# Kernel tuning notes

Measured on AMD Instinct MI355X. Metric: run time of the kernel, lower is better.

Reference implementation:

```python
import jax, jax.numpy as jnp
import numpy as np
from jax import lax

B, T, V, D, H, NH = 32, 2048, 50257, 512, 512, 2
HD = D // NH
EPS_ATTN = 1e-6
EPS_LN = 1e-5


def setup_inputs() -> dict:
    key = jax.random.key(0)
    ks = jax.random.split(key, 16)
    s = 0.02
    n = lambda k, shape: jax.random.normal(k, shape, jnp.float32) * s
    return {
        'input_ids': jax.random.randint(ks[0], (B, T), 0, V),
        'emb': n(ks[1], (V, D)),
        'Wq': n(ks[2], (D, D)), 'Wk': n(ks[3], (D, D)), 'Wv': n(ks[4], (D, D)),
        'Wo': n(ks[5], (D, D)),  # present in module, unused in forward (kept for parity)
        'Wg': n(ks[6], (D, D)), 'bg': jnp.zeros((D,), jnp.float32),
        'W_in': n(ks[7], (H, D)), 'b_in': jnp.zeros((H,), jnp.float32),
        'W_h': n(ks[8], (H, H)),
        'log_tau': jnp.zeros((H,), jnp.float32),
        'log_dt': jnp.zeros((H,), jnp.float32),
        'W_zx': n(ks[9], (H, D)), 'b_zx': jnp.zeros((H,), jnp.float32),
        'W_zh': n(ks[10], (H, H)),
        'fast_W': jnp.zeros((H, H), jnp.float32),  # registered buffer, starts at zero
        'ln_g': jnp.ones((H,), jnp.float32), 'ln_b': jnp.zeros((H,), jnp.float32),
        'Wlm': n(ks[11], (V, H)), 'blm': jnp.zeros((V,), jnp.float32),
    }


def _phi(x):
    return jax.nn.elu(x) + 1.0


def _forward(input_ids, emb, Wq, Wk, Wv, Wo, Wg, bg, W_in, b_in, W_h, log_tau,
             log_dt, W_zx, b_zx, W_zh, fast_W, ln_g, ln_b, Wlm, blm):
    x = emb[input_ids]  # [B,T,D]

    # LiquidSelfAttention (diagonal linear attention, as written in the source)
    q = _phi((x @ Wq.T).reshape(B, T, NH, HD))
    k = _phi((x @ Wk.T).reshape(B, T, NH, HD))
    v = (x @ Wv.T).reshape(B, T, NH, HD)
    k_sum = k.sum(axis=1)                       # [B,NH,HD]
    kv_sum = (k * v).sum(axis=1)                # einsum('bthd,bthd->bhd')
    num = jnp.einsum('bthd,bhd->bth', q, kv_sum)[..., None]   # [B,T,NH,1]
    den = jnp.einsum('bthd,bhd->bth', q, k_sum)[..., None] + EPS_ATTN
    out = jnp.broadcast_to(num / den, (B, T, NH, HD)).reshape(B, T, D)
    gate = jax.nn.sigmoid(x @ Wg.T + bg)
    x = gate * out + (1.0 - gate) * x           # [B,T,D]

    # Liquid-GRU recurrence with fast-weight term
    tau = jnp.exp(log_tau)
    dt = jnp.exp(log_dt)
    h0 = jnp.zeros((B, H), x.dtype)

    def step(carry, x_t):
        h, _ = carry
        u = x_t @ W_in.T + b_in + h @ W_h.T
        f = jnp.tanh(u)
        h_liquid = h + dt * (f - tau * h)
        z = jax.nn.sigmoid(x_t @ W_zx.T + b_zx + h @ W_zh.T)
        slow_h = (1.0 - z) * h + z * h_liquid
        h_next = slow_h + h @ fast_W
        return (h_next, h), None

    (h_last, h_prev), _ = lax.scan(step, (h0, h0), jnp.swapaxes(x, 0, 1))
    pred_error = h_last - h_prev  # last-step prediction error (T >= 2)

    # LayerNorm (dropout is identity in eval)
    mu = h_last.mean(axis=-1, keepdims=True)
    var = ((h_last - mu) ** 2).mean(axis=-1, keepdims=True)
    h = (h_last - mu) * lax.rsqrt(var + EPS_LN) * ln_g + ln_b

    logits = h @ Wlm.T + blm
    pred_error_norm = jnp.sqrt(jnp.mean(pred_error ** 2))
    return logits, h, pred_error_norm


def reference(input_ids, emb, Wq, Wk, Wv, Wo, Wg, bg, W_in, b_in, W_h, log_tau,
              log_dt, W_zx, b_zx, W_zh, fast_W, ln_g, ln_b, Wlm, blm):
    return _forward(input_ids, emb, Wq, Wk, Wv, Wo, Wg, bg, W_in, b_in, W_h,
                    log_tau, log_dt, W_zx, b_zx, W_zh, fast_W, ln_g, ln_b, Wlm, blm)
```

## Files before the change

### kernel.cpp

```cpp
#include <hip/hip_runtime.h>
#include <cstdint>
#include <cstddef>


#define B_ 32
#define T_ 2048
#define V_ 50257
#define D_ 512
#define H_ 512
#define NH_ 2
#define BT_ (B_*T_)

typedef float f32x4 __attribute__((ext_vector_type(4)));

#define OFF_X0    ((size_t)0)
#define OFF_X1    (OFF_X0 + (size_t)BT_*D_*4)
#define OFF_XZ    (OFF_X1 + (size_t)BT_*D_*4)
#define OFF_SMALL (OFF_XZ + (size_t)BT_*D_*4)
#define OFF_RBUF  (OFF_SMALL)
#define OFF_KSUM  (OFF_RBUF + (size_t)BT_*NH_*2*4)
#define OFF_KVSUM (OFF_KSUM + (size_t)B_*D_*4)
#define OFF_FLAGS (OFF_KVSUM + (size_t)B_*D_*4)
#define OFF_HBUF  (OFF_FLAGS + 16384)
#define OFF_HLN   (OFF_HBUF + (size_t)2*B_*H_*4)
#define ZERO_F4   ((OFF_HBUF - OFF_SMALL) / 16)

__device__ __forceinline__ float phi_f(float x) {
  return x > 0.f ? x + 1.f : expf(x);
}
__device__ __forceinline__ float sigm_f(float x) {
  return 1.f / (1.f + expf(-x));
}

__global__ __launch_bounds__(256) void zero_k(float4* __restrict__ p, int n) {
  int i = blockIdx.x * 256 + threadIdx.x;
  if (i < n) p[i] = make_float4(0.f, 0.f, 0.f, 0.f);
}

__global__ __launch_bounds__(256) void fillnan_k(uint4* __restrict__ p) {
  size_t i = (size_t)blockIdx.x * 256 + threadIdx.x;
  uint4 v;
  v.x = 0x7FC00000u; v.y = 0x7FC00000u; v.z = 0x7FC00000u; v.w = 0x7FC00000u;
  p[i] = v;
}

__global__ __launch_bounds__(256) void embed_k(const int* __restrict__ ids,
                                               const float* __restrict__ emb,
                                               float* __restrict__ x0) {
  size_t idx = (size_t)blockIdx.x * 256 + threadIdx.x;
  int row = (int)(idx >> 7), c = (int)(idx & 127);
  int id = ids[row];
  ((float4*)x0)[idx] = ((const float4*)emb)[(size_t)id * 128 + c];
}

template<int MODE>
__global__ __launch_bounds__(256, 2) void gemm_k(
    const float* __restrict__ X, const float* __restrict__ W0,
    const float* __restrict__ W1, const float* __restrict__ bias,
    const float* __restrict__ aux0, const float* __restrict__ aux1,
    float* __restrict__ out0, float* __restrict__ out1) {
  constexpr bool KV = (MODE == 0);
  __shared__ float Xs[32][68];
  __shared__ float Ws[32][68];
  __shared__ float Ws2[KV ? 32 : 1][68];
  const int tid = threadIdx.x;
  const int m0 = blockIdx.x * 64, n0 = blockIdx.y * 64;
  const int tm = tid >> 4, tn = tid & 15;
  const int lr = tid >> 3;
  const int lc = (tid & 7) * 4;
  float acc[4][4] = {};
  float acc2[KV ? 4 : 1][4] = {};

  for (int k0 = 0; k0 < 512; k0 += 32) {
    const float4 xa = *(const float4*)&X[(size_t)(m0 + lr) * 512 + k0 + lc];
    const float4 xb = *(const float4*)&X[(size_t)(m0 + 32 + lr) * 512 + k0 + lc];
    const float4 wa = *(const float4*)&W0[(size_t)(n0 + lr) * 512 + k0 + lc];
    const float4 wb = *(const float4*)&W0[(size_t)(n0 + 32 + lr) * 512 + k0 + lc];
    float4 va, vb;
    if constexpr (KV) {
      va = *(const float4*)&W1[(size_t)(n0 + lr) * 512 + k0 + lc];
      vb = *(const float4*)&W1[(size_t)(n0 + 32 + lr) * 512 + k0 + lc];
    }
    __syncthreads();
    Xs[lc+0][lr] = xa.x; Xs[lc+1][lr] = xa.y; Xs[lc+2][lr] = xa.z; Xs[lc+3][lr] = xa.w;
    Xs[lc+0][lr+32] = xb.x; Xs[lc+1][lr+32] = xb.y; Xs[lc+2][lr+32] = xb.z; Xs[lc+3][lr+32] = xb.w;
    Ws[lc+0][lr] = wa.x; Ws[lc+1][lr] = wa.y; Ws[lc+2][lr] = wa.z; Ws[lc+3][lr] = wa.w;
    Ws[lc+0][lr+32] = wb.x; Ws[lc+1][lr+32] = wb.y; Ws[lc+2][lr+32] = wb.z; Ws[lc+3][lr+32] = wb.w;
    if constexpr (KV) {
      Ws2[lc+0][lr] = va.x; Ws2[lc+1][lr] = va.y; Ws2[lc+2][lr] = va.z; Ws2[lc+3][lr] = va.w;
      Ws2[lc+0][lr+32] = vb.x; Ws2[lc+1][lr+32] = vb.y; Ws2[lc+2][lr+32] = vb.z; Ws2[lc+3][lr+32] = vb.w;
    }
    __syncthreads();
    #pragma unroll
    for (int kk = 0; kk < 32; ++kk) {
      float4 xv = *(const float4*)&Xs[kk][tm * 4];
      float4 wv = *(const float4*)&Ws[kk][tn * 4];
      const float* xf = (const float*)&xv;
      const float* wf = (const float*)&wv;
      #pragma unroll
      for (int i = 0; i < 4; ++i)
        #pragma unroll
        for (int j = 0; j < 4; ++j)
          acc[i][j] += xf[i] * wf[j];
      if constexpr (KV) {
        float4 wv2 = *(const float4*)&Ws2[kk][tn * 4];
        const float* w2 = (const float*)&wv2;
        #pragma unroll
        for (int i = 0; i < 4; ++i)
          #pragma unroll
          for (int j = 0; j < 4; ++j)
            acc2[i][j] += xf[i] * w2[j];
      }
    }
  }

  if constexpr (MODE == 0) {
    __syncthreads();
    float* red = &Xs[0][0];
    if (tid < 128) red[tid] = 0.f;
    __syncthreads();
    #pragma unroll
    for (int j = 0; j < 4; ++j) {
      float ks = 0.f, kvs = 0.f;
      #pragma unroll
      for (int i = 0; i < 4; ++i) {
        float kk_ = phi_f(acc[i][j]);
        ks += kk_;
        kvs += kk_ * acc2[i][j];
      }
      atomicAdd(&red[(tn * 4 + j) * 2 + 0], ks);
      atomicAdd(&red[(tn * 4 + j) * 2 + 1], kvs);
    }
    __syncthreads();
    if (tid < 64) {
      int b = m0 >> 11;
      atomicAdd(&out0[b * 512 + n0 + tid], red[tid * 2 + 0]);
      atomicAdd(&out1[b * 512 + n0 + tid], red[tid * 2 + 1]);
    }
  } else if constexpr (MODE == 1) {
    int b = m0 >> 11;
    float kvv[4], ksv[4];
    #pragma unroll
    for (int j = 0; j < 4; ++j) {
      int n = n0 + tn * 4 + j;
      kvv[j] = aux0[b * 512 + n];
      ksv[j] = aux1[b * 512 + n];
    }
    __syncthreads();
    float* red = &Xs[0][0];
    if (tid < 128) red[tid] = 0.f;
    __syncthreads();
    #pragma unroll
    for (int i = 0; i < 4; ++i) {
      float np = 0.f, dp = 0.f;
      #pragma unroll
      for (int j = 0; j < 4; ++j) {
        float q = phi_f(acc[i][j]);
        np += q * kvv[j];
        dp += q * ksv[j];
      }
      atomicAdd(&red[(tm * 4 + i) * 2 + 0], np);
      atomicAdd(&red[(tm * 4 + i) * 2 + 1], dp);
    }
    __syncthreads();
    if (tid < 64) {
      int m = m0 + tid, h = n0 >> 8;
      atomicAdd(&out0[((size_t)m * 2 + h) * 2 + 0], red[tid * 2 + 0]);
      atomicAdd(&out0[((size_t)m * 2 + h) * 2 + 1], red[tid * 2 + 1]);
    }
  } else if constexpr (MODE == 2) {
    int h = n0 >> 8;
    #pragma unroll
    for (int i = 0; i < 4; ++i) {
      int m = m0 + tm * 4 + i;
      float rn = aux0[((size_t)m * 2 + h) * 2 + 0];
      float rd = aux0[((size_t)m * 2 + h) * 2 + 1];
      float r = rn / (rd + 1e-6f);
      float4 x0v = *(const float4*)&aux1[(size_t)m * 512 + n0 + tn * 4];
      const float* xf = (const float*)&x0v;
      float4 o;
      float* of = (float*)&o;
      #pragma unroll
      for (int j = 0; j < 4; ++j) {
        int n = n0 + tn * 4 + j;
        float g = sigm_f(acc[i][j] + bias[n]);
        of[j] = g * r + (1.f - g) * xf[j];
      }
      *(float4*)&out0[(size_t)m * 512 + n0 + tn * 4] = o;
    }
  } else {
    #pragma unroll
    for (int i = 0; i < 4; ++i) {
      int m = m0 + tm * 4 + i;
      float4 o;
      float* of = (float*)&o;
      #pragma unroll
      for (int j = 0; j < 4; ++j)
        of[j] = acc[i][j] + bias[n0 + tn * 4 + j];
      *(float4*)&out0[(size_t)m * 512 + n0 + tn * 4] = o;
    }
  }
}


#define ISSUE8(h0,h1,h2,h3,h4_,h5,h6,h7,ptr) \
  asm volatile( \
    "global_load_dwordx4 %0, %8, off sc0 sc1\n\t" \
    "global_load_dwordx4 %1, %8, off offset:16 sc0 sc1\n\t" \
    "global_load_dwordx4 %2, %8, off offset:32 sc0 sc1\n\t" \
    "global_load_dwordx4 %3, %8, off offset:48 sc0 sc1\n\t" \
    "global_load_dwordx4 %4, %8, off offset:64 sc0 sc1\n\t" \
    "global_load_dwordx4 %5, %8, off offset:80 sc0 sc1\n\t" \
    "global_load_dwordx4 %6, %8, off offset:96 sc0 sc1\n\t" \
    "global_load_dwordx4 %7, %8, off offset:112 sc0 sc1" \
    : "=v"(h0), "=v"(h1), "=v"(h2), "=v"(h3), \
      "=v"(h4_), "=v"(h5), "=v"(h6), "=v"(h7) \
    : "v"(ptr))

#define WAIT_TIE(h0,h1,h2,h3,h4_,h5,h6,h7) \
  asm volatile("s_waitcnt vmcnt(0)" \
    : "+v"(h0), "+v"(h1), "+v"(h2), "+v"(h3), \
      "+v"(h4_), "+v"(h5), "+v"(h6), "+v"(h7))

__global__ __launch_bounds__(1024) void scan_k(
    const float* __restrict__ xin, const float* __restrict__ xz,
    const float* __restrict__ Wh, const float* __restrict__ Wzh,
    const float* __restrict__ fastW,
    const float* __restrict__ log_tau, const float* __restrict__ log_dt,
    float* __restrict__ hist) {
  __shared__ float red[16][64][3];
  __shared__ __align__(16) float h_lds[2][64];
  const int tid = threadIdx.x;
  const int b = blockIdx.x >> 3;
  const int q = blockIdx.x & 7;
  const int w = tid >> 6;
  const int lane = tid & 63;
  const int jg = q * 64 + lane;
  const int kb = w * 32;
  const int src = w >> 1;

  f32x4 wh[8], wz[8], fw[8];
  #pragma unroll
  for (int i = 0; i < 8; ++i) {
    wh[i] = *(const f32x4*)&Wh[(size_t)jg * 512 + kb + i * 4];
    wz[i] = *(const f32x4*)&Wzh[(size_t)jg * 512 + kb + i * 4];
    f32x4 tv;
    tv.x = fastW[(size_t)(kb + i * 4 + 0) * 512 + jg];
    tv.y = fastW[(size_t)(kb + i * 4 + 1) * 512 + jg];
    tv.z = fastW[(size_t)(kb + i * 4 + 2) * 512 + jg];
    tv.w = fastW[(size_t)(kb + i * 4 + 3) * 512 + jg];
    fw[i] = tv;
  }
  bool fwz = true;
  #pragma unroll
  for (int i = 0; i < 8; ++i)
    fwz = fwz & (fw[i].x == 0.f) & (fw[i].y == 0.f) & (fw[i].z == 0.f) & (fw[i].w == 0.f);

  const float dtv = expf(log_dt[jg]);
  const float tauv = expf(log_tau[jg]);
  float hold = 0.f;
  float pxin = 0.f, pxz = 0.f;
  if (w == 0) {
    const float* xip = xin + (size_t)b * T_ * 512 + jg;
    const float* xzp = xz + (size_t)b * T_ * 512 + jg;
    asm volatile("global_load_dword %0, %2, off\n\t"
                 "global_load_dword %1, %3, off"
                 : "=v"(pxin), "=v"(pxz) : "v"(xip), "v"(xzp));
  }

  for (int t = 0; t < T_; ++t) {
    float am0 = 0.f, am1 = 0.f, am2 = 0.f;
    if (t != 0) {
      f32x4 hv[8];
      if (src == q) {
        const float* hl = &h_lds[t & 1][kb & 63];
        #pragma unroll
        for (int i = 0; i < 8; ++i) hv[i] = *(const f32x4*)(hl + i * 4);
      } else {
        const float* hp = hist + (size_t)(t - 1) * (B_ * H_) + b * 512 + kb;
        ISSUE8(hv[0], hv[1], hv[2], hv[3], hv[4], hv[5], hv[6], hv[7], hp);
        while (true) {
          WAIT_TIE(hv[0], hv[1], hv[2], hv[3], hv[4], hv[5], hv[6], hv[7]);
          f32x4 sv = hv[0] + hv[1] + hv[2] + hv[3] + hv[4] + hv[5] + hv[6] + hv[7];
          float sred = sv.x + sv.y + sv.z + sv.w;
          if ((__float_as_uint(sred) & 0x7F800000u) != 0x7F800000u) break;
          ISSUE8(hv[0], hv[1], hv[2], hv[3], hv[4], hv[5], hv[6], hv[7], hp);
        }
      }
      #pragma unroll
      for (int i = 0; i < 8; ++i) {
        f32x4 h4 = hv[i];
        am0 += wh[i].x * h4.x + wh[i].y * h4.y + wh[i].z * h4.z + wh[i].w * h4.w;
        am1 += wz[i].x * h4.x + wz[i].y * h4.y + wz[i].z * h4.z + wz[i].w * h4.w;
      }
      if (!fwz) {
        #pragma unroll
        for (int i = 0; i < 8; ++i) {
          f32x4 h4 = hv[i];
          am2 += fw[i].x * h4.x + fw[i].y * h4.y + fw[i].z * h4.z + fw[i].w * h4.w;
        }
      }
    }
    red[w][lane][0] = am0;
    red[w][lane][1] = am1;
    red[w][lane][2] = am2;
    __syncthreads();
    if (w == 0) {
      float s0 = 0.f, s1 = 0.f, s2 = 0.f;
      #pragma unroll
      for (int ww = 0; ww < 16; ++ww) {
        s0 += red[ww][lane][0];
        s1 += red[ww][lane][1];
        s2 += red[ww][lane][2];
      }
      asm volatile("s_waitcnt vmcnt(0)" : "+v"(pxin), "+v"(pxz));
      float u = pxin + s0;
      float f = tanhf(u);
      float hl2 = hold + dtv * (f - tauv * hold);
      float zv = sigm_f(pxz + s1);
      float slow = (1.f - zv) * hold + zv * hl2;
      float hnv = slow + s2;
      hold = hnv;
      h_lds[(t + 1) & 1][lane] = hnv;
      float* dst = hist + (size_t)t * (B_ * H_) + b * 512 + jg;
      asm volatile("global_store_dword %0, %1, off sc0 sc1" :: "v"(dst), "v"(hnv) : "memory");
      if (t + 1 < T_) {
        const float* xip = xin + ((size_t)b * T_ + (t + 1)) * 512 + jg;
        const float* xzp = xz + ((size_t)b * T_ + (t + 1)) * 512 + jg;
        asm volatile("global_load_dword %0, %2, off\n\t"
                     "global_load_dword %1, %3, off"
                     : "=v"(pxin), "=v"(pxz) : "v"(xip), "v"(xzp));
      }
    }
    __syncthreads();
  }
}

__global__ __launch_bounds__(256) void pred_k(const float* __restrict__ hA,
                                              const float* __restrict__ hB,
                                              float* __restrict__ out) {
  const int tid = threadIdx.x;
  float s = 0.f;
  for (int i = tid; i < H_ * B_; i += 256) {
    float a = __hip_atomic_load((const float*)&hA[i], __ATOMIC_RELAXED, __HIP_MEMORY_SCOPE_AGENT);
    float b = __hip_atomic_load((const float*)&hB[i], __ATOMIC_RELAXED, __HIP_MEMORY_SCOPE_AGENT);
    float d = a - b;
    s += d * d;
  }
  #pragma unroll
  for (int m = 1; m < 64; m <<= 1) s += __shfl_xor(s, m, 64);
  __shared__ float r8[4];
  if ((tid & 63) == 0) r8[tid >> 6] = s;
  __syncthreads();
  if (tid == 0) out[0] = sqrtf((r8[0] + r8[1] + r8[2] + r8[3]) * (1.f / (H_ * B_)));
}

__global__ __launch_bounds__(256) void ln_k(const float* __restrict__ h0,
                                            const float* __restrict__ g,
                                            const float* __restrict__ be,
                                            float* __restrict__ hln,
                                            float* __restrict__ outh) {
  const int b = blockIdx.x, tid = threadIdx.x;
  float v0 = __hip_atomic_load((const float*)&h0[b * 512 + tid], __ATOMIC_RELAXED, __HIP_MEMORY_SCOPE_AGENT);
  float v1 = __hip_atomic_load((const float*)&h0[b * 512 + tid + 256], __ATOMIC_RELAXED, __HIP_MEMORY_SCOPE_AGENT);
  float s = v0 + v1;
  #pragma unroll
  for (int m = 1; m < 64; m <<= 1) s += __shfl_xor(s, m, 64);
  __shared__ float r8[8];
  if ((tid & 63) == 0) r8[tid >> 6] = s;
  __syncthreads();
  float mu = (r8[0] + r8[1] + r8[2] + r8[3]) * (1.f / 512.f);
  float d0 = v0 - mu, d1 = v1 - mu;
  float s2 = d0 * d0 + d1 * d1;
  #pragma unroll
  for (int m = 1; m < 64; m <<= 1) s2 += __shfl_xor(s2, m, 64);
  if ((tid & 63) == 0) r8[4 + (tid >> 6)] = s2;
  __syncthreads();
  float var = (r8[4] + r8[5] + r8[6] + r8[7]) * (1.f / 512.f);
  float inv = rsqrtf(var + 1e-5f);
  float y0 = d0 * inv * g[tid] + be[tid];
  float y1 = d1 * inv * g[tid + 256] + be[tid + 256];
  hln[b * 512 + tid] = y0;
  hln[b * 512 + tid + 256] = y1;
  outh[b * 512 + tid] = y0;
  outh[b * 512 + tid + 256] = y1;
}

__global__ __launch_bounds__(256, 2) void logits_k(const float* __restrict__ hln,
                                                   const float* __restrict__ Wlm,
                                                   const float* __restrict__ blm,
                                                   float* __restrict__ out) {
  __shared__ float hs[32 * 513];
  const int tid = threadIdx.x;
  for (int idx = tid; idx < 16384; idx += 256) {
    int b = idx >> 9, k = idx & 511;
    hs[b * 513 + k] = hln[idx];
  }
  __syncthreads();
  const int lane = tid & 63, w = tid >> 6;
  const int b = lane & 31, kh = lane >> 5;
  const float* hb = &hs[b * 513 + kh * 256];
  const int vbase = blockIdx.x * 64 + w * 16;
  for (int r4 = 0; r4 < 16; r4 += 4) {
    int v = vbase + r4;
    int v0i = (v + 0 < V_) ? v + 0 : V_ - 1;
    int v1i = (v + 1 < V_) ? v + 1 : V_ - 1;
    int v2i = (v + 2 < V_) ? v + 2 : V_ - 1;
    int v3i = (v + 3 < V_) ? v + 3 : V_ - 1;
    const float4* w0 = (const float4*)&Wlm[(size_t)v0i * 512 + kh * 256];
    const float4* w1 = (const float4*)&Wlm[(size_t)v1i * 512 + kh * 256];
    const float4* w2 = (const float4*)&Wlm[(size_t)v2i * 512 + kh * 256];
    const float4* w3 = (const float4*)&Wlm[(size_t)v3i * 512 + kh * 256];
    float a0 = 0.f, a1 = 0.f, a2 = 0.f, a3 = 0.f;
    #pragma unroll 8
    for (int q = 0; q < 64; ++q) {
      float h0 = hb[q * 4 + 0], h1 = hb[q * 4 + 1], h2 = hb[q * 4 + 2], h3 = hb[q * 4 + 3];
      float4 x;
      x = w0[q]; a0 += x.x * h0 + x.y * h1 + x.z * h2 + x.w * h3;
      x = w1[q]; a1 += x.x * h0 + x.y * h1 + x.z * h2 + x.w * h3;
      x = w2[q]; a2 += x.x * h0 + x.y * h1 + x.z * h2 + x.w * h3;
      x = w3[q]; a3 += x.x * h0 + x.y * h1 + x.z * h2 + x.w * h3;
    }
    a0 += __shfl_xor(a0, 32, 64);
    a1 += __shfl_xor(a1, 32, 64);
    a2 += __shfl_xor(a2, 32, 64);
    a3 += __shfl_xor(a3, 32, 64);
    if (lane < 32) {
      if (v + 0 < V_) out[(size_t)b * V_ + v + 0] = a0 + blm[v + 0];
      if (v + 1 < V_) out[(size_t)b * V_ + v + 1] = a1 + blm[v + 1];
      if (v + 2 < V_) out[(size_t)b * V_ + v + 2] = a2 + blm[v + 2];
      if (v + 3 < V_) out[(size_t)b * V_ + v + 3] = a3 + blm[v + 3];
    }
  }
}

extern "C" void kernel_launch(void* const* d_in, const int* in_sizes, int n_in,
                              void* d_out, int out_size, void* d_ws, size_t ws_size,
                              hipStream_t stream) {
  const int*   ids     = (const int*)d_in[0];
  const float* emb     = (const float*)d_in[1];
  const float* Wq      = (const float*)d_in[2];
  const float* Wk      = (const float*)d_in[3];
  const float* Wv      = (const float*)d_in[4];
  const float* Wg      = (const float*)d_in[6];
  const float* bg      = (const float*)d_in[7];
  const float* W_in    = (const float*)d_in[8];
  const float* b_in    = (const float*)d_in[9];
  const float* W_h     = (const float*)d_in[10];
  const float* log_tau = (const float*)d_in[11];
  const float* log_dt  = (const float*)d_in[12];
  const float* W_zx    = (const float*)d_in[13];
  const float* b_zx    = (const float*)d_in[14];
  const float* W_zh    = (const float*)d_in[15];
  const float* fast_W  = (const float*)d_in[16];
  const float* ln_g    = (const float*)d_in[17];
  const float* ln_b    = (const float*)d_in[18];
  const float* Wlm     = (const float*)d_in[19];
  const float* blm     = (const float*)d_in[20];

  char* ws = (char*)d_ws;
  float* x0    = (float*)(ws + OFF_X0);
  float* x1    = (float*)(ws + OFF_X1);
  float* xzb   = (float*)(ws + OFF_XZ);
  float* rbuf  = (float*)(ws + OFF_RBUF);
  float* ksum  = (float*)(ws + OFF_KSUM);
  float* kvsum = (float*)(ws + OFF_KVSUM);
  float* hln   = (float*)(ws + OFF_HLN);
  float* out   = (float*)d_out;

  const int nzero = (int)ZERO_F4;
  zero_k<<<dim3((nzero + 255) / 256), dim3(256), 0, stream>>>((float4*)(ws + OFF_SMALL), nzero);
  embed_k<<<dim3(BT_ * 128 / 256), dim3(256), 0, stream>>>(ids, emb, x0);

  dim3 gg(BT_ / 64, 8);
  gemm_k<0><<<gg, dim3(256), 0, stream>>>(x0, Wk, Wv, nullptr, nullptr, nullptr, ksum, kvsum);
  gemm_k<1><<<gg, dim3(256), 0, stream>>>(x0, Wq, nullptr, nullptr, kvsum, ksum, rbuf, nullptr);
  gemm_k<2><<<gg, dim3(256), 0, stream>>>(x0, Wg, nullptr, bg, rbuf, x0, x1, nullptr);
  gemm_k<3><<<gg, dim3(256), 0, stream>>>(x1, W_in, nullptr, b_in, nullptr, nullptr, x0, nullptr);
  gemm_k<3><<<gg, dim3(256), 0, stream>>>(x1, W_zx, nullptr, b_zx, nullptr, nullptr, xzb, nullptr);

  fillnan_k<<<dim3(BT_ * D_ / 4 / 256), dim3(256), 0, stream>>>((uint4*)x1);

  scan_k<<<dim3(256), dim3(1024), 0, stream>>>(x0, xzb, W_h, W_zh, fast_W, log_tau, log_dt, x1);

  float* hlast = x1 + (size_t)2047 * (B_ * H_);
  float* hprev = x1 + (size_t)2046 * (B_ * H_);
  pred_k<<<dim3(1), dim3(256), 0, stream>>>(hlast, hprev, out + (size_t)B_ * V_ + (size_t)B_ * H_);
  ln_k<<<dim3(32), dim3(256), 0, stream>>>(hlast, ln_g, ln_b, hln, out + (size_t)B_ * V_);
  logits_k<<<dim3((V_ + 63) / 64), dim3(256), 0, stream>>>(hln, Wlm, blm, out);
}
```

Measured before the change: 7.691 ms.

## Exchange partial matvec sums via triple-buffered slots instead of full hidden-state history

```diff
diff --git a/kernel.cpp b/kernel.cpp
--- a/kernel.cpp
+++ b/kernel.cpp
@@ -25,6 +25,9 @@
 #define OFF_HLN   (OFF_HBUF + (size_t)2*B_*H_*4)
 #define ZERO_F4   ((OFF_HBUF - OFF_SMALL) / 16)
 
+#define MATS_MAX 3
+#define SLOT_F   (MATS_MAX*8*512)
+
 __device__ __forceinline__ float phi_f(float x) {
   return x > 0.f ? x + 1.f : expf(x);
 }
@@ -42,6 +45,13 @@
   uint4 v;
   v.x = 0x7FC00000u; v.y = 0x7FC00000u; v.z = 0x7FC00000u; v.w = 0x7FC00000u;
   p[i] = v;
+}
+
+__global__ __launch_bounds__(256) void fwnz_k(const float* __restrict__ fw,
+                                              int* __restrict__ flag) {
+  int i = (blockIdx.x * 256 + threadIdx.x) * 4;
+  float4 v = *(const float4*)&fw[i];
+  if (v.x != 0.f || v.y != 0.f || v.z != 0.f || v.w != 0.f) atomicOr(flag, 1);
 }
 
 __global__ __launch_bounds__(256) void embed_k(const int* __restrict__ ids,
@@ -203,117 +213,87 @@
 }
 
 
-#define ISSUE8(h0,h1,h2,h3,h4_,h5,h6,h7,ptr) \
-  asm volatile( \
-    "global_load_dwordx4 %0, %8, off sc0 sc1\n\t" \
-    "global_load_dwordx4 %1, %8, off offset:16 sc0 sc1\n\t" \
-    "global_load_dwordx4 %2, %8, off offset:32 sc0 sc1\n\t" \
-    "global_load_dwordx4 %3, %8, off offset:48 sc0 sc1\n\t" \
-    "global_load_dwordx4 %4, %8, off offset:64 sc0 sc1\n\t" \
-    "global_load_dwordx4 %5, %8, off offset:80 sc0 sc1\n\t" \
-    "global_load_dwordx4 %6, %8, off offset:96 sc0 sc1\n\t" \
-    "global_load_dwordx4 %7, %8, off offset:112 sc0 sc1" \
-    : "=v"(h0), "=v"(h1), "=v"(h2), "=v"(h3), \
-      "=v"(h4_), "=v"(h5), "=v"(h6), "=v"(h7) \
-    : "v"(ptr))
-
-#define WAIT_TIE(h0,h1,h2,h3,h4_,h5,h6,h7) \
-  asm volatile("s_waitcnt vmcnt(0)" \
-    : "+v"(h0), "+v"(h1), "+v"(h2), "+v"(h3), \
-      "+v"(h4_), "+v"(h5), "+v"(h6), "+v"(h7))
+#define LOADWAIT(dst, ptr) \
+  asm volatile("global_load_dword %0, %1, off sc0 sc1\n\t" \
+               "s_waitcnt vmcnt(0)" \
+               : "=v"(dst) : "v"(ptr) : "memory")
+#define PSTORE(ptr, val) \
+  asm volatile("global_store_dword %0, %1, off sc0 sc1" :: "v"(ptr), "v"(val) : "memory")
 
 __global__ __launch_bounds__(1024) void scan_k(
     const float* __restrict__ xin, const float* __restrict__ xz,
     const float* __restrict__ Wh, const float* __restrict__ Wzh,
     const float* __restrict__ fastW,
     const float* __restrict__ log_tau, const float* __restrict__ log_dt,
-    float* __restrict__ hist) {
-  __shared__ float red[16][64][3];
-  __shared__ __align__(16) float h_lds[2][64];
+    float* __restrict__ slots, float* __restrict__ hlast,
+    float* __restrict__ hprev, const int* __restrict__ fwflag) {
+  __shared__ float red[24][64];
+  __shared__ __align__(16) float h_lds[64];
   const int tid = threadIdx.x;
   const int b = blockIdx.x >> 3;
-  const int q = blockIdx.x & 7;
-  const int w = tid >> 6;
-  const int lane = tid & 63;
-  const int jg = q * 64 + lane;
-  const int kb = w * 32;
-  const int src = w >> 1;
-
-  f32x4 wh[8], wz[8], fw[8];
+  const int o = blockIdx.x & 7;
+  const int w = tid >> 6, lane = tid & 63;
+  const int j = tid & 511, mat = tid >> 9;
+  const int mats = (fwflag[0] != 0) ? 3 : 2;
+
+  const float* Wsel = mat ? Wzh : Wh;
+  f32x4 wv[16];
   #pragma unroll
-  for (int i = 0; i < 8; ++i) {
-    wh[i] = *(const f32x4*)&Wh[(size_t)jg * 512 + kb + i * 4];
-    wz[i] = *(const f32x4*)&Wzh[(size_t)jg * 512 + kb + i * 4];
-    f32x4 tv;
-    tv.x = fastW[(size_t)(kb + i * 4 + 0) * 512 + jg];
-    tv.y = fastW[(size_t)(kb + i * 4 + 1) * 512 + jg];
-    tv.z = fastW[(size_t)(kb + i * 4 + 2) * 512 + jg];
-    tv.w = fastW[(size_t)(kb + i * 4 + 3) * 512 + jg];
-    fw[i] = tv;
-  }
-  bool fwz = true;
-  #pragma unroll
-  for (int i = 0; i < 8; ++i)
-    fwz = fwz & (fw[i].x == 0.f) & (fw[i].y == 0.f) & (fw[i].z == 0.f) & (fw[i].w == 0.f);
-
-  const float dtv = expf(log_dt[jg]);
-  const float tauv = expf(log_tau[jg]);
-  float hold = 0.f;
-  float pxin = 0.f, pxz = 0.f;
+  for (int i = 0; i < 16; ++i)
+    wv[i] = *(const f32x4*)&Wsel[(size_t)j * 512 + o * 64 + i * 4];
+
+  const int col = o * 64 + lane;
+  const float* xinb = xin + (size_t)b * T_ * 512 + col;
+  const float* xzbp = xz + (size_t)b * T_ * 512 + col;
+  float dtv = 0.f, tauv = 0.f, hold = 0.f, pxin = 0.f, pxz = 0.f;
   if (w == 0) {
-    const float* xip = xin + (size_t)b * T_ * 512 + jg;
-    const float* xzp = xz + (size_t)b * T_ * 512 + jg;
-    asm volatile("global_load_dword %0, %2, off\n\t"
-                 "global_load_dword %1, %3, off"
-                 : "=v"(pxin), "=v"(pxz) : "v"(xip), "v"(xzp));
-  }
+    dtv = expf(log_dt[col]);
+    tauv = expf(log_tau[col]);
+    pxin = xinb[0];
+    pxz = xzbp[0];
+  }
+
+  const float qnan = __int_as_float(0x7FC00000);
 
   for (int t = 0; t < T_; ++t) {
-    float am0 = 0.f, am1 = 0.f, am2 = 0.f;
     if (t != 0) {
-      f32x4 hv[8];
-      if (src == q) {
-        const float* hl = &h_lds[t & 1][kb & 63];
+      const float* base = slots + ((size_t)(t % 3) * 32 + b) * SLOT_F;
+      const float* cp = base + w * 512 + col;
+      float pv;
+      while (true) {
+        LOADWAIT(pv, cp);
+        if (__ballot((__float_as_uint(pv) & 0x7F800000u) != 0x7F800000u) == ~0ull) break;
+      }
+      red[w][lane] = pv;
+      if (mats == 3 && w < 8) {
+        const float* cp2 = base + (16 + w) * 512 + col;
+        float pv2;
+        while (true) {
+          LOADWAIT(pv2, cp2);
+          if (__ballot((__float_as_uint(pv2) & 0x7F800000u) != 0x7F800000u) == ~0ull) break;
+        }
+        red[16 + w][lane] = pv2;
+      }
+    } else {
+      red[w][lane] = 0.f;
+      if (mats == 3 && w < 8) red[16 + w][lane] = 0.f;
+    }
+    __syncthreads();
+
+    float* nfb = slots + ((size_t)((t + 2) % 3) * 32 + b) * SLOT_F;
+    if (w != 0) {
+      if (t >= 1) {
+        PSTORE(nfb + (mat * 8 + o) * 512 + j, qnan);
+        if (mats == 3 && mat == 0) PSTORE(nfb + (16 + o) * 512 + j, qnan);
+      }
+    } else {
+      float s0 = 0.f, s1 = 0.f, s2 = 0.f;
+      #pragma unroll
+      for (int oo = 0; oo < 8; ++oo) { s0 += red[oo][lane]; s1 += red[8 + oo][lane]; }
+      if (mats == 3) {
         #pragma unroll
-        for (int i = 0; i < 8; ++i) hv[i] = *(const f32x4*)(hl + i * 4);
-      } else {
-        const float* hp = hist + (size_t)(t - 1) * (B_ * H_) + b * 512 + kb;
-        ISSUE8(hv[0], hv[1], hv[2], hv[3], hv[4], hv[5], hv[6], hv[7], hp);
-        while (true) {
-          WAIT_TIE(hv[0], hv[1], hv[2], hv[3], hv[4], hv[5], hv[6], hv[7]);
-          f32x4 sv = hv[0] + hv[1] + hv[2] + hv[3] + hv[4] + hv[5] + hv[6] + hv[7];
-          float sred = sv.x + sv.y + sv.z + sv.w;
-          if ((__float_as_uint(sred) & 0x7F800000u) != 0x7F800000u) break;
-          ISSUE8(hv[0], hv[1], hv[2], hv[3], hv[4], hv[5], hv[6], hv[7], hp);
-        }
-      }
-      #pragma unroll
-      for (int i = 0; i < 8; ++i) {
-        f32x4 h4 = hv[i];
-        am0 += wh[i].x * h4.x + wh[i].y * h4.y + wh[i].z * h4.z + wh[i].w * h4.w;
-        am1 += wz[i].x * h4.x + wz[i].y * h4.y + wz[i].z * h4.z + wz[i].w * h4.w;
-      }
-      if (!fwz) {
-        #pragma unroll
-        for (int i = 0; i < 8; ++i) {
-          f32x4 h4 = hv[i];
-          am2 += fw[i].x * h4.x + fw[i].y * h4.y + fw[i].z * h4.z + fw[i].w * h4.w;
-        }
-      }
-    }
-    red[w][lane][0] = am0;
-    red[w][lane][1] = am1;
-    red[w][lane][2] = am2;
-    __syncthreads();
-    if (w == 0) {
-      float s0 = 0.f, s1 = 0.f, s2 = 0.f;
-      #pragma unroll
-      for (int ww = 0; ww < 16; ++ww) {
-        s0 += red[ww][lane][0];
-        s1 += red[ww][lane][1];
-        s2 += red[ww][lane][2];
-      }
-      asm volatile("s_waitcnt vmcnt(0)" : "+v"(pxin), "+v"(pxz));
+        for (int oo = 0; oo < 8; ++oo) s2 += red[16 + oo][lane];
+      }
       float u = pxin + s0;
       float f = tanhf(u);
       float hl2 = hold + dtv * (f - tauv * hold);
@@ -321,18 +301,33 @@
       float slow = (1.f - zv) * hold + zv * hl2;
       float hnv = slow + s2;
       hold = hnv;
-      h_lds[(t + 1) & 1][lane] = hnv;
-      float* dst = hist + (size_t)t * (B_ * H_) + b * 512 + jg;
-      asm volatile("global_store_dword %0, %1, off sc0 sc1" :: "v"(dst), "v"(hnv) : "memory");
+      h_lds[lane] = hnv;
+      if (t == 2046) hprev[b * 512 + col] = hnv;
+      if (t == 2047) hlast[b * 512 + col] = hnv;
+      if (t >= 1) {
+        PSTORE(nfb + o * 512 + j, qnan);
+        if (mats == 3) PSTORE(nfb + (16 + o) * 512 + j, qnan);
+      }
       if (t + 1 < T_) {
-        const float* xip = xin + ((size_t)b * T_ + (t + 1)) * 512 + jg;
-        const float* xzp = xz + ((size_t)b * T_ + (t + 1)) * 512 + jg;
-        asm volatile("global_load_dword %0, %2, off\n\t"
-                     "global_load_dword %1, %3, off"
-                     : "=v"(pxin), "=v"(pxz) : "v"(xip), "v"(xzp));
-      }
-    }
-    __syncthreads();
+        pxin = xinb[(size_t)(t + 1) * 512];
+        pxz = xzbp[(size_t)(t + 1) * 512];
+      }
+    }
+    __syncthreads();
+
+    float acc = 0.f, acc2 = 0.f;
+    #pragma unroll
+    for (int kk = 0; kk < 16; ++kk) {
+      f32x4 h4 = *(const f32x4*)&h_lds[kk * 4];
+      acc += wv[kk].x * h4.x + wv[kk].y * h4.y + wv[kk].z * h4.z + wv[kk].w * h4.w;
+    }
+    if (mats == 3 && mat == 0) {
+      for (int kk = 0; kk < 64; ++kk)
+        acc2 += fastW[(size_t)(o * 64 + kk) * 512 + j] * h_lds[kk];
+    }
+    float* dstb = slots + ((size_t)((t + 1) % 3) * 32 + b) * SLOT_F;
+    PSTORE(dstb + (mat * 8 + o) * 512 + j, acc);
+    if (mats == 3 && mat == 0) PSTORE(dstb + (16 + o) * 512 + j, acc2);
   }
 }
 
@@ -342,8 +337,8 @@
   const int tid = threadIdx.x;
   float s = 0.f;
   for (int i = tid; i < H_ * B_; i += 256) {
-    float a = __hip_atomic_load((const float*)&hA[i], __ATOMIC_RELAXED, __HIP_MEMORY_SCOPE_AGENT);
-    float b = __hip_atomic_load((const float*)&hB[i], __ATOMIC_RELAXED, __HIP_MEMORY_SCOPE_AGENT);
+    float a = hA[i];
+    float b = hB[i];
     float d = a - b;
     s += d * d;
   }
@@ -361,8 +356,8 @@
                                             float* __restrict__ hln,
                                             float* __restrict__ outh) {
   const int b = blockIdx.x, tid = threadIdx.x;
-  float v0 = __hip_atomic_load((const float*)&h0[b * 512 + tid], __ATOMIC_RELAXED, __HIP_MEMORY_SCOPE_AGENT);
-  float v1 = __hip_atomic_load((const float*)&h0[b * 512 + tid + 256], __ATOMIC_RELAXED, __HIP_MEMORY_SCOPE_AGENT);
+  float v0 = h0[b * 512 + tid];
+  float v1 = h0[b * 512 + tid + 256];
   float s = v0 + v1;
   #pragma unroll
   for (int m = 1; m < 64; m <<= 1) s += __shfl_xor(s, m, 64);
@@ -465,6 +460,9 @@
   float* rbuf  = (float*)(ws + OFF_RBUF);
   float* ksum  = (float*)(ws + OFF_KSUM);
   float* kvsum = (float*)(ws + OFF_KVSUM);
+  int*   fwfl  = (int*)(ws + OFF_FLAGS);
+  float* hlast = (float*)(ws + OFF_HBUF);
+  float* hprev = (float*)(ws + OFF_HBUF) + (size_t)B_ * H_;
   float* hln   = (float*)(ws + OFF_HLN);
   float* out   = (float*)d_out;
 
@@ -479,12 +477,13 @@
   gemm_k<3><<<gg, dim3(256), 0, stream>>>(x1, W_in, nullptr, b_in, nullptr, nullptr, x0, nullptr);
   gemm_k<3><<<gg, dim3(256), 0, stream>>>(x1, W_zx, nullptr, b_zx, nullptr, nullptr, xzb, nullptr);
 
-  fillnan_k<<<dim3(BT_ * D_ / 4 / 256), dim3(256), 0, stream>>>((uint4*)x1);
-
-  scan_k<<<dim3(256), dim3(1024), 0, stream>>>(x0, xzb, W_h, W_zh, fast_W, log_tau, log_dt, x1);
-
-  float* hlast = x1 + (size_t)2047 * (B_ * H_);
-  float* hprev = x1 + (size_t)2046 * (B_ * H_);
+  fwnz_k<<<dim3(512 * 512 / 1024), dim3(256), 0, stream>>>(fast_W, fwfl);
+
+  fillnan_k<<<dim3(3 * 32 * SLOT_F / 4 / 256), dim3(256), 0, stream>>>((uint4*)x1);
+
+  scan_k<<<dim3(256), dim3(1024), 0, stream>>>(
+      x0, xzb, W_h, W_zh, fast_W, log_tau, log_dt, x1, hlast, hprev, fwfl);
+
   pred_k<<<dim3(1), dim3(256), 0, stream>>>(hlast, hprev, out + (size_t)B_ * V_ + (size_t)B_ * H_);
   ln_k<<<dim3(32), dim3(256), 0, stream>>>(hlast, ln_g, ln_b, hln, out + (size_t)B_ * V_);
   logits_k<<<dim3((V_ + 63) / 64), dim3(256), 0, stream>>>(hln, Wlm, blm, out);
```

Result: slower. 16.09 ms (+109.1%).

## Replace FP32 LDS-tiled GEMMs with bf16 MFMA GEMMs and fuse W_in/W_zx projections

Applied to the files above, without the earlier changes.

```diff
diff --git a/kernel.cpp b/kernel.cpp
--- a/kernel.cpp
+++ b/kernel.cpp
@@ -12,6 +12,8 @@
 #define BT_ (B_*T_)
 
 typedef float f32x4 __attribute__((ext_vector_type(4)));
+typedef short bf16x8 __attribute__((ext_vector_type(8)));
+typedef unsigned int u32x4 __attribute__((ext_vector_type(4)));
 
 #define OFF_X0    ((size_t)0)
 #define OFF_X1    (OFF_X0 + (size_t)BT_*D_*4)
@@ -32,6 +34,17 @@
   return 1.f / (1.f + expf(-x));
 }
 
+__device__ __forceinline__ bf16x8 cvt8(float4 a, float4 b) {
+  unsigned int r0, r1, r2, r3;
+  asm("v_cvt_pk_bf16_f32 %0, %1, %2" : "=v"(r0) : "v"(a.x), "v"(a.y));
+  asm("v_cvt_pk_bf16_f32 %0, %1, %2" : "=v"(r1) : "v"(a.z), "v"(a.w));
+  asm("v_cvt_pk_bf16_f32 %0, %1, %2" : "=v"(r2) : "v"(b.x), "v"(b.y));
+  asm("v_cvt_pk_bf16_f32 %0, %1, %2" : "=v"(r3) : "v"(b.z), "v"(b.w));
+  union { u32x4 u; bf16x8 h; } z;
+  z.u = (u32x4){r0, r1, r2, r3};
+  return z.h;
+}
+
 __global__ __launch_bounds__(256) void zero_k(float4* __restrict__ p, int n) {
   int i = blockIdx.x * 256 + threadIdx.x;
   if (i < n) p[i] = make_float4(0.f, 0.f, 0.f, 0.f);
@@ -54,150 +67,131 @@
 }
 
 template<int MODE>
-__global__ __launch_bounds__(256, 2) void gemm_k(
+__global__ __launch_bounds__(256, 2) void mgemm_k(
     const float* __restrict__ X, const float* __restrict__ W0,
-    const float* __restrict__ W1, const float* __restrict__ bias,
+    const float* __restrict__ W1, const float* __restrict__ bias0,
+    const float* __restrict__ bias1,
     const float* __restrict__ aux0, const float* __restrict__ aux1,
     float* __restrict__ out0, float* __restrict__ out1) {
-  constexpr bool KV = (MODE == 0);
-  __shared__ float Xs[32][68];
-  __shared__ float Ws[32][68];
-  __shared__ float Ws2[KV ? 32 : 1][68];
+  constexpr bool DUAL = (MODE == 0 || MODE == 3);
   const int tid = threadIdx.x;
-  const int m0 = blockIdx.x * 64, n0 = blockIdx.y * 64;
-  const int tm = tid >> 4, tn = tid & 15;
-  const int lr = tid >> 3;
-  const int lc = (tid & 7) * 4;
-  float acc[4][4] = {};
-  float acc2[KV ? 4 : 1][4] = {};
+  const int w = tid >> 6, lane = tid & 63;
+  const int n0 = blockIdx.x * 64;
+  const int m0 = blockIdx.y * 64;
+  const int ko8 = (lane >> 4) * 8;
+
+  const float* xp = X + (size_t)(m0 + w * 16 + (lane & 15)) * 512 + ko8;
+  const float* w0p = W0 + (size_t)(n0 + (lane & 15)) * 512 + ko8;
+  const float* w1p = DUAL ? (W1 + (size_t)(n0 + (lane & 15)) * 512 + ko8) : nullptr;
+
+  f32x4 acc[4], acc2[DUAL ? 4 : 1];
+  #pragma unroll
+  for (int f = 0; f < 4; ++f) { acc[f] = (f32x4){0.f,0.f,0.f,0.f}; }
+  #pragma unroll
+  for (int f = 0; f < (DUAL ? 4 : 1); ++f) { acc2[f] = (f32x4){0.f,0.f,0.f,0.f}; }
 
   for (int k0 = 0; k0 < 512; k0 += 32) {
-    const float4 xa = *(const float4*)&X[(size_t)(m0 + lr) * 512 + k0 + lc];
-    const float4 xb = *(const float4*)&X[(size_t)(m0 + 32 + lr) * 512 + k0 + lc];
-    const float4 wa = *(const float4*)&W0[(size_t)(n0 + lr) * 512 + k0 + lc];
-    const float4 wb = *(const float4*)&W0[(size_t)(n0 + 32 + lr) * 512 + k0 + lc];
-    float4 va, vb;
-    if constexpr (KV) {
-      va = *(const float4*)&W1[(size_t)(n0 + lr) * 512 + k0 + lc];
-      vb = *(const float4*)&W1[(size_t)(n0 + 32 + lr) * 512 + k0 + lc];
-    }
+    float4 xa = *(const float4*)(xp + k0);
+    float4 xb = *(const float4*)(xp + k0 + 4);
+    bf16x8 av = cvt8(xa, xb);
+    #pragma unroll
+    for (int f = 0; f < 4; ++f) {
+      float4 wa = *(const float4*)(w0p + (size_t)f * 16 * 512 + k0);
+      float4 wb = *(const float4*)(w0p + (size_t)f * 16 * 512 + k0 + 4);
+      bf16x8 bv = cvt8(wa, wb);
+      acc[f] = __builtin_amdgcn_mfma_f32_16x16x32_bf16(av, bv, acc[f], 0, 0, 0);
+      if constexpr (DUAL) {
+        float4 va = *(const float4*)(w1p + (size_t)f * 16 * 512 + k0);
+        float4 vb = *(const float4*)(w1p + (size_t)f * 16 * 512 + k0 + 4);
+        bf16x8 bv2 = cvt8(va, vb);
+        acc2[f] = __builtin_amdgcn_mfma_f32_16x16x32_bf16(av, bv2, acc2[f], 0, 0, 0);
+      }
+    }
+  }
+
+  if constexpr (MODE == 0) {
+    __shared__ float kred[128];
+    if (tid < 128) kred[tid] = 0.f;
     __syncthreads();
-    Xs[lc+0][lr] = xa.x; Xs[lc+1][lr] = xa.y; Xs[lc+2][lr] = xa.z; Xs[lc+3][lr] = xa.w;
-    Xs[lc+0][lr+32] = xb.x; Xs[lc+1][lr+32] = xb.y; Xs[lc+2][lr+32] = xb.z; Xs[lc+3][lr+32] = xb.w;
-    Ws[lc+0][lr] = wa.x; Ws[lc+1][lr] = wa.y; Ws[lc+2][lr] = wa.z; Ws[lc+3][lr] = wa.w;
-    Ws[lc+0][lr+32] = wb.x; Ws[lc+1][lr+32] = wb.y; Ws[lc+2][lr+32] = wb.z; Ws[lc+3][lr+32] = wb.w;
-    if constexpr (KV) {
-      Ws2[lc+0][lr] = va.x; Ws2[lc+1][lr] = va.y; Ws2[lc+2][lr] = va.z; Ws2[lc+3][lr] = va.w;
-      Ws2[lc+0][lr+32] = vb.x; Ws2[lc+1][lr+32] = vb.y; Ws2[lc+2][lr+32] = vb.z; Ws2[lc+3][lr+32] = vb.w;
-    }
-    __syncthreads();
-    #pragma unroll
-    for (int kk = 0; kk < 32; ++kk) {
-      float4 xv = *(const float4*)&Xs[kk][tm * 4];
-      float4 wv = *(const float4*)&Ws[kk][tn * 4];
-      const float* xf = (const float*)&xv;
-      const float* wf = (const float*)&wv;
-      #pragma unroll
-      for (int i = 0; i < 4; ++i)
-        #pragma unroll
-        for (int j = 0; j < 4; ++j)
-          acc[i][j] += xf[i] * wf[j];
-      if constexpr (KV) {
-        float4 wv2 = *(const float4*)&Ws2[kk][tn * 4];
-        const float* w2 = (const float*)&wv2;
-        #pragma unroll
-        for (int i = 0; i < 4; ++i)
-          #pragma unroll
-          for (int j = 0; j < 4; ++j)
-            acc2[i][j] += xf[i] * w2[j];
-      }
-    }
-  }
-
-  if constexpr (MODE == 0) {
-    __syncthreads();
-    float* red = &Xs[0][0];
-    if (tid < 128) red[tid] = 0.f;
-    __syncthreads();
-    #pragma unroll
-    for (int j = 0; j < 4; ++j) {
+    #pragma unroll
+    for (int f = 0; f < 4; ++f) {
       float ks = 0.f, kvs = 0.f;
       #pragma unroll
-      for (int i = 0; i < 4; ++i) {
-        float kk_ = phi_f(acc[i][j]);
-        ks += kk_;
-        kvs += kk_ * acc2[i][j];
-      }
-      atomicAdd(&red[(tn * 4 + j) * 2 + 0], ks);
-      atomicAdd(&red[(tn * 4 + j) * 2 + 1], kvs);
+      for (int r = 0; r < 4; ++r) {
+        float kk = phi_f(acc[f][r]);
+        ks += kk;
+        kvs += kk * acc2[f][r];
+      }
+      ks += __shfl_xor(ks, 16, 64);  ks += __shfl_xor(ks, 32, 64);
+      kvs += __shfl_xor(kvs, 16, 64); kvs += __shfl_xor(kvs, 32, 64);
+      if ((lane >> 4) == 0) {
+        atomicAdd(&kred[(16 * f + lane) * 2 + 0], ks);
+        atomicAdd(&kred[(16 * f + lane) * 2 + 1], kvs);
+      }
     }
     __syncthreads();
     if (tid < 64) {
       int b = m0 >> 11;
-      atomicAdd(&out0[b * 512 + n0 + tid], red[tid * 2 + 0]);
-      atomicAdd(&out1[b * 512 + n0 + tid], red[tid * 2 + 1]);
+      atomicAdd(&out0[b * 512 + n0 + tid], kred[tid * 2 + 0]);
+      atomicAdd(&out1[b * 512 + n0 + tid], kred[tid * 2 + 1]);
     }
   } else if constexpr (MODE == 1) {
-    int b = m0 >> 11;
-    float kvv[4], ksv[4];
-    #pragma unroll
-    for (int j = 0; j < 4; ++j) {
-      int n = n0 + tn * 4 + j;
-      kvv[j] = aux0[b * 512 + n];
-      ksv[j] = aux1[b * 512 + n];
-    }
-    __syncthreads();
-    float* red = &Xs[0][0];
-    if (tid < 128) red[tid] = 0.f;
-    __syncthreads();
-    #pragma unroll
-    for (int i = 0; i < 4; ++i) {
-      float np = 0.f, dp = 0.f;
-      #pragma unroll
-      for (int j = 0; j < 4; ++j) {
-        float q = phi_f(acc[i][j]);
-        np += q * kvv[j];
-        dp += q * ksv[j];
-      }
-      atomicAdd(&red[(tm * 4 + i) * 2 + 0], np);
-      atomicAdd(&red[(tm * 4 + i) * 2 + 1], dp);
-    }
-    __syncthreads();
-    if (tid < 64) {
-      int m = m0 + tid, h = n0 >> 8;
-      atomicAdd(&out0[((size_t)m * 2 + h) * 2 + 0], red[tid * 2 + 0]);
-      atomicAdd(&out0[((size_t)m * 2 + h) * 2 + 1], red[tid * 2 + 1]);
+    int bq = m0 >> 11, h = n0 >> 8;
+    float np[4] = {0.f,0.f,0.f,0.f}, dp[4] = {0.f,0.f,0.f,0.f};
+    #pragma unroll
+    for (int f = 0; f < 4; ++f) {
+      int n = n0 + 16 * f + (lane & 15);
+      float kv = aux0[bq * 512 + n];
+      float ksv = aux1[bq * 512 + n];
+      #pragma unroll
+      for (int r = 0; r < 4; ++r) {
+        float q = phi_f(acc[f][r]);
+        np[r] += q * kv;
+        dp[r] += q * ksv;
+      }
+    }
+    #pragma unroll
+    for (int r = 0; r < 4; ++r) {
+      #pragma unroll
+      for (int m = 1; m < 16; m <<= 1) {
+        np[r] += __shfl_xor(np[r], m, 64);
+        dp[r] += __shfl_xor(dp[r], m, 64);
+      }
+    }
+    if ((lane & 15) == 0) {
+      #pragma unroll
+      for (int r = 0; r < 4; ++r) {
+        int m = m0 + w * 16 + (lane >> 4) * 4 + r;
+        atomicAdd(&out0[((size_t)m * 2 + h) * 2 + 0], np[r]);
+        atomicAdd(&out0[((size_t)m * 2 + h) * 2 + 1], dp[r]);
+      }
     }
   } else if constexpr (MODE == 2) {
     int h = n0 >> 8;
     #pragma unroll
-    for (int i = 0; i < 4; ++i) {
-      int m = m0 + tm * 4 + i;
+    for (int r = 0; r < 4; ++r) {
+      int m = m0 + w * 16 + (lane >> 4) * 4 + r;
       float rn = aux0[((size_t)m * 2 + h) * 2 + 0];
       float rd = aux0[((size_t)m * 2 + h) * 2 + 1];
-      float r = rn / (rd + 1e-6f);
-      float4 x0v = *(const float4*)&aux1[(size_t)m * 512 + n0 + tn * 4];
-      const float* xf = (const float*)&x0v;
-      float4 o;
-      float* of = (float*)&o;
-      #pragma unroll
-      for (int j = 0; j < 4; ++j) {
-        int n = n0 + tn * 4 + j;
-        float g = sigm_f(acc[i][j] + bias[n]);
-        of[j] = g * r + (1.f - g) * xf[j];
-      }
-      *(float4*)&out0[(size_t)m * 512 + n0 + tn * 4] = o;
+      float rv = rn / (rd + 1e-6f);
+      #pragma unroll
+      for (int f = 0; f < 4; ++f) {
+        int n = n0 + 16 * f + (lane & 15);
+        float g = sigm_f(acc[f][r] + bias0[n]);
+        float xv = aux1[(size_t)m * 512 + n];
+        out0[(size_t)m * 512 + n] = g * rv + (1.f - g) * xv;
+      }
     }
   } else {
     #pragma unroll
-    for (int i = 0; i < 4; ++i) {
-      int m = m0 + tm * 4 + i;
-      float4 o;
-      float* of = (float*)&o;
-      #pragma unroll
-      for (int j = 0; j < 4; ++j)
-        of[j] = acc[i][j] + bias[n0 + tn * 4 + j];
-      *(float4*)&out0[(size_t)m * 512 + n0 + tn * 4] = o;
+    for (int r = 0; r < 4; ++r) {
+      int m = m0 + w * 16 + (lane >> 4) * 4 + r;
+      #pragma unroll
+      for (int f = 0; f < 4; ++f) {
+        int n = n0 + 16 * f + (lane & 15);
+        out0[(size_t)m * 512 + n] = acc[f][r] + bias0[n];
+        out1[(size_t)m * 512 + n] = acc2[f][r] + bias1[n];
+      }
     }
   }
 }
@@ -472,12 +466,11 @@
   zero_k<<<dim3((nzero + 255) / 256), dim3(256), 0, stream>>>((float4*)(ws + OFF_SMALL), nzero);
   embed_k<<<dim3(BT_ * 128 / 256), dim3(256), 0, stream>>>(ids, emb, x0);
 
-  dim3 gg(BT_ / 64, 8);
-  gemm_k<0><<<gg, dim3(256), 0, stream>>>(x0, Wk, Wv, nullptr, nullptr, nullptr, ksum, kvsum);
-  gemm_k<1><<<gg, dim3(256), 0, stream>>>(x0, Wq, nullptr, nullptr, kvsum, ksum, rbuf, nullptr);
-  gemm_k<2><<<gg, dim3(256), 0, stream>>>(x0, Wg, nullptr, bg, rbuf, x0, x1, nullptr);
-  gemm_k<3><<<gg, dim3(256), 0, stream>>>(x1, W_in, nullptr, b_in, nullptr, nullptr, x0, nullptr);
-  gemm_k<3><<<gg, dim3(256), 0, stream>>>(x1, W_zx, nullptr, b_zx, nullptr, nullptr, xzb, nullptr);
+  dim3 gg(8, BT_ / 64);
+  mgemm_k<0><<<gg, dim3(256), 0, stream>>>(x0, Wk, Wv, nullptr, nullptr, nullptr, nullptr, ksum, kvsum);
+  mgemm_k<1><<<gg, dim3(256), 0, stream>>>(x0, Wq, nullptr, nullptr, nullptr, kvsum, ksum, rbuf, nullptr);
+  mgemm_k<2><<<gg, dim3(256), 0, stream>>>(x0, Wg, nullptr, bg, nullptr, rbuf, x0, x1, nullptr);
+  mgemm_k<3><<<gg, dim3(256), 0, stream>>>(x1, W_in, W_zx, b_in, b_zx, nullptr, nullptr, x0, xzb);
 
   fillnan_k<<<dim3(BT_ * D_ / 4 / 256), dim3(256), 0, stream>>>((uint4*)x1);
 
```

After: 7.704 ms. No clear change (+0.2%).
